# Kernel tuning notes

Measured on AMD Instinct MI355X. Metric: run time of the kernel, lower is better.

The kernel has to match this reference:

```python
import jax, jax.numpy as jnp
import numpy as np

B, IN_CAPS, IN_DIM = 64, 512, 128
NUM_CAPS, DIM_CAPS, NUM_ROUTING = 32, 32, 3


def squash(x, axis=-1):
    sn = jnp.sum(x * x, axis=axis, keepdims=True)
    return (sn / (1.0 + sn)) * x / (jnp.sqrt(sn) + 1e-8)


def setup_inputs() -> dict:
    key = jax.random.key(0)
    k1, k2, k3 = jax.random.split(key, 3)
    input_tensor = jax.random.normal(k1, (B, IN_CAPS, IN_DIM), dtype=jnp.float32)
    W = 0.001 * jax.random.normal(k2, (NUM_CAPS, IN_DIM, DIM_CAPS), dtype=jnp.float32)
    b0 = jax.random.uniform(k3, (B, NUM_CAPS, IN_CAPS, 1), dtype=jnp.float32)
    return {"input_tensor": input_tensor, "W": W, "b0": b0}


def reference(input_tensor, W, b0):
    # u_hat: (B, num_caps, in_caps, dim_caps)
    u_hat = jnp.einsum('bid,ndc->bnic', input_tensor, W)
    temp_u_hat = jax.lax.stop_gradient(u_hat)
    b = b0
    for _ in range(NUM_ROUTING - 1):
        c = jax.nn.softmax(b, axis=1)            # (B, num_caps, in_caps, 1)
        s = jnp.sum(c * temp_u_hat, axis=2)      # (B, num_caps, dim_caps)
        v = squash(s)
        uv = jnp.einsum('bnic,bnc->bni', temp_u_hat, v)[..., None]
        b = b + uv
    c = jax.nn.softmax(b, axis=1)
    s = jnp.sum(c * u_hat, axis=2)
    return squash(s)                             # (B, num_caps, dim_caps)
```

## Files before the change

### kernel.cpp

```cpp
#include <hip/hip_runtime.h>
#include <math.h>

#define IC 512
#define KD 128
#define NC 32
#define DC 32
#define NTHR 512

typedef __attribute__((ext_vector_type(8))) short bf16x8;
typedef __attribute__((ext_vector_type(4))) float f32x4;

__device__ __forceinline__ unsigned short f2bf(float f) {
    unsigned u = __builtin_bit_cast(unsigned, f);
    return (unsigned short)((u + 0x7fffu + ((u >> 16) & 1u)) >> 16);
}
__device__ __forceinline__ float bf2f(unsigned short h) {
    unsigned u = ((unsigned)h) << 16;
    return __builtin_bit_cast(float, u);
}
#define MFMA(a, b, c) __builtin_amdgcn_mfma_f32_16x16x32_bf16(a, b, c, 0, 0, 0)

__global__ __launch_bounds__(NTHR, 1)
void capsmfma(const float* __restrict__ x_g, const float* __restrict__ W_g,
              const float* __restrict__ b0_g, float* __restrict__ out_g,
              unsigned short* __restrict__ xT_g)
{
    __shared__ __align__(16) unsigned short uA[512 * 34];
    __shared__ __align__(16) float s_s[NC * KD];
    __shared__ __align__(16) unsigned short wv_s[NC * 136];

    const int t = threadIdx.x, b = blockIdx.x;
    const int w = t >> 6, l = t & 63;
    const float* __restrict__ xb = x_g + (size_t)b * IC * KD;
    unsigned short* __restrict__ xTb = xT_g + (size_t)b * KD * IC;

    {
        float* tile = (float*)uA;
        for (int c = 0; c < 8; ++c) {
            for (int rep = 0; rep < 4; ++rep) {
                int v = t + rep * NTHR;
                int i = v >> 5, kq = v & 31;
                float4 val = *(const float4*)(xb + (size_t)(c * 64 + i) * KD + (kq << 2));
                float* d = tile + i * 133 + (kq << 2);
                d[0] = val.x; d[1] = val.y; d[2] = val.z; d[3] = val.w;
            }
            __syncthreads();
            {
                const int xk = t >> 2, iseg = t & 3;
                unsigned q[8];
                #pragma unroll
                for (int j = 0; j < 8; ++j) {
                    unsigned short lo = f2bf(tile[(iseg * 16 + 2 * j) * 133 + xk]);
                    unsigned short hi = f2bf(tile[(iseg * 16 + 2 * j + 1) * 133 + xk]);
                    q[j] = (unsigned)lo | ((unsigned)hi << 16);
                }
                unsigned short* dst = xTb + (size_t)xk * IC + c * 64 + iseg * 16;
                float4 o0 = {__builtin_bit_cast(float, q[0]), __builtin_bit_cast(float, q[1]),
                             __builtin_bit_cast(float, q[2]), __builtin_bit_cast(float, q[3])};
                float4 o1 = {__builtin_bit_cast(float, q[4]), __builtin_bit_cast(float, q[5]),
                             __builtin_bit_cast(float, q[6]), __builtin_bit_cast(float, q[7])};
                *(float4*)(dst) = o0;
                *(float4*)(dst + 8) = o1;
            }
            __syncthreads();
        }
    }

    float bb[NC];
    #pragma unroll
    for (int n = 0; n < NC; ++n)
        bb[n] = b0_g[((size_t)(b * NC + n)) * IC + t];

    unsigned short* stage = uA;
    unsigned short* c_bf  = uA;

    for (int r = 0; r < 3; ++r) {
        if (r > 0) {
            f32x4 acc[4][2];
            #pragma unroll
            for (int m4 = 0; m4 < 4; ++m4)
                #pragma unroll
                for (int nt = 0; nt < 2; ++nt) acc[m4][nt] = (f32x4){0.f, 0.f, 0.f, 0.f};
            const int lm = l & 15, kg = l >> 4;
            for (int kt = 0; kt < 4; ++kt) {
                const int xk = kt * 32 + kg * 8;
                bf16x8 bfr0 = *(const bf16x8*)(const void*)(wv_s + (0 * 16 + lm) * 136 + xk);
                bf16x8 bfr1 = *(const bf16x8*)(const void*)(wv_s + (1 * 16 + lm) * 136 + xk);
                #pragma unroll
                for (int m4 = 0; m4 < 4; ++m4) {
                    const int i = (4 * w + m4) * 16 + lm;
                    float4 xa = *(const float4*)(xb + (size_t)i * KD + xk);
                    float4 xc = *(const float4*)(xb + (size_t)i * KD + xk + 4);
                    bf16x8 afr;
                    afr[0] = (short)f2bf(xa.x); afr[1] = (short)f2bf(xa.y);
                    afr[2] = (short)f2bf(xa.z); afr[3] = (short)f2bf(xa.w);
                    afr[4] = (short)f2bf(xc.x); afr[5] = (short)f2bf(xc.y);
                    afr[6] = (short)f2bf(xc.z); afr[7] = (short)f2bf(xc.w);
                    acc[m4][0] = MFMA(afr, bfr0, acc[m4][0]);
                    acc[m4][1] = MFMA(afr, bfr1, acc[m4][1]);
                }
            }
            #pragma unroll
            for (int m4 = 0; m4 < 4; ++m4)
                #pragma unroll
                for (int nt = 0; nt < 2; ++nt)
                    #pragma unroll
                    for (int reg = 0; reg < 4; ++reg) {
                        const int i = (4 * w + m4) * 16 + kg * 4 + reg;
                        const int n = nt * 16 + lm;
                        stage[i * 34 + n] = f2bf(acc[m4][nt][reg]);
                    }
            __syncthreads();
            #pragma unroll
            for (int n = 0; n < NC; ++n) bb[n] += bf2f(stage[t * 34 + n]);
            __syncthreads();
        }

        {
            float m = bb[0];
            #pragma unroll
            for (int n = 1; n < NC; ++n) m = fmaxf(m, bb[n]);
            float e[NC], sum = 0.f;
            #pragma unroll
            for (int n = 0; n < NC; ++n) { e[n] = __expf(bb[n] - m); sum += e[n]; }
            const float inv = 1.f / sum;
            #pragma unroll
            for (int n = 0; n < NC; ++n) c_bf[n * 520 + t] = f2bf(e[n] * inv);
        }
        __syncthreads();

        {
            f32x4 acc2[2];
            acc2[0] = (f32x4){0.f, 0.f, 0.f, 0.f};
            acc2[1] = (f32x4){0.f, 0.f, 0.f, 0.f};
            const int lm = l & 15, kg = l >> 4;
            for (int kt = 0; kt < 16; ++kt) {
                const int i0 = kt * 32 + kg * 8;
                float4 raw = *(const float4*)(xTb + (size_t)(w * 16 + lm) * IC + i0);
                bf16x8 bfr = __builtin_bit_cast(bf16x8, raw);
                #pragma unroll
                for (int mt = 0; mt < 2; ++mt) {
                    bf16x8 afr = *(const bf16x8*)(const void*)(c_bf + (mt * 16 + lm) * 520 + i0);
                    acc2[mt] = MFMA(afr, bfr, acc2[mt]);
                }
            }
            #pragma unroll
            for (int mt = 0; mt < 2; ++mt)
                #pragma unroll
                for (int reg = 0; reg < 4; ++reg) {
                    const int n = mt * 16 + kg * 4 + reg;
                    const int xk = w * 16 + lm;
                    s_s[n * KD + (xk & 96) + ((xk + 4 * n) & 31)] = acc2[mt][reg];
                }
        }
        __syncthreads();

        {
            const int n = t >> 4, dp = t & 15;
            const float* __restrict__ Wn = W_g + (size_t)n * KD * DC;
            float s0 = 0.f, s1 = 0.f;
            #pragma unroll 8
            for (int k = 0; k < KD; ++k) {
                const float sv = s_s[n * KD + (k & 96) + ((k + 4 * n) & 31)];
                const float2 wp = *(const float2*)(Wn + k * DC + (dp << 1));
                s0 += sv * wp.x; s1 += sv * wp.y;
            }
            float sn = s0 * s0 + s1 * s1;
            sn += __shfl_xor(sn, 1); sn += __shfl_xor(sn, 2);
            sn += __shfl_xor(sn, 4); sn += __shfl_xor(sn, 8);
            const float fac = sn / ((1.f + sn) * (sqrtf(sn) + 1e-8f));
            const float v0 = s0 * fac, v1 = s1 * fac;
            if (r == 2) {
                float* o = out_g + ((size_t)(b * NC + n)) * DC + (dp << 1);
                o[0] = v0; o[1] = v1;
            } else {
                float vv[DC];
                const int base = (l >> 4) << 4;
                #pragma unroll
                for (int dd = 0; dd < 16; ++dd) {
                    vv[2 * dd]     = __shfl(v0, base + dd);
                    vv[2 * dd + 1] = __shfl(v1, base + dd);
                }
                #pragma unroll
                for (int kk = 0; kk < 8; ++kk) {
                    const int k = dp * 8 + kk;
                    const float* __restrict__ wr = Wn + k * DC;
                    float a = 0.f;
                    #pragma unroll
                    for (int dd = 0; dd < DC; ++dd) a += wr[dd] * vv[dd];
                    wv_s[n * 136 + k] = f2bf(a);
                }
                __syncthreads();
            }
        }
    }
}

extern "C" void kernel_launch(void* const* d_in, const int* in_sizes, int n_in,
                              void* d_out, int out_size, void* d_ws, size_t ws_size,
                              hipStream_t stream) {
    const float* x  = (const float*)d_in[0];
    const float* W  = (const float*)d_in[1];
    const float* b0 = (const float*)d_in[2];
    float* out = (float*)d_out;
    unsigned short* xT = (unsigned short*)d_ws;
    capsmfma<<<64, NTHR, 0, stream>>>(x, W, b0, out, xT);
}
```

Baseline: 156.3 us.

## Double block size and keep routing logits in MFMA accumulator layout

```diff
diff --git a/kernel.cpp b/kernel.cpp
--- a/kernel.cpp
+++ b/kernel.cpp
@@ -5,7 +5,7 @@
 #define KD 128
 #define NC 32
 #define DC 32
-#define NTHR 512
+#define NTHR 1024
 
 typedef __attribute__((ext_vector_type(8))) short bf16x8;
 typedef __attribute__((ext_vector_type(4))) float f32x4;
@@ -14,184 +14,177 @@
     unsigned u = __builtin_bit_cast(unsigned, f);
     return (unsigned short)((u + 0x7fffu + ((u >> 16) & 1u)) >> 16);
 }
-__device__ __forceinline__ float bf2f(unsigned short h) {
-    unsigned u = ((unsigned)h) << 16;
-    return __builtin_bit_cast(float, u);
-}
 #define MFMA(a, b, c) __builtin_amdgcn_mfma_f32_16x16x32_bf16(a, b, c, 0, 0, 0)
 
 __global__ __launch_bounds__(NTHR, 1)
 void capsmfma(const float* __restrict__ x_g, const float* __restrict__ W_g,
               const float* __restrict__ b0_g, float* __restrict__ out_g,
-              unsigned short* __restrict__ xT_g)
+              unsigned short* __restrict__ xT_g, unsigned short* __restrict__ xb_g)
 {
-    __shared__ __align__(16) unsigned short uA[512 * 34];
+    __shared__ __align__(16) float uni[8512];
     __shared__ __align__(16) float s_s[NC * KD];
     __shared__ __align__(16) unsigned short wv_s[NC * 136];
+    __shared__ __align__(16) float v_s[NC * 33];
 
     const int t = threadIdx.x, b = blockIdx.x;
-    const int w = t >> 6, l = t & 63;
+    const int w = t >> 6, l = t & 63, lm = l & 15, kg = (l >> 4) & 3;
     const float* __restrict__ xb = x_g + (size_t)b * IC * KD;
     unsigned short* __restrict__ xTb = xT_g + (size_t)b * KD * IC;
-
-    {
-        float* tile = (float*)uA;
-        for (int c = 0; c < 8; ++c) {
-            for (int rep = 0; rep < 4; ++rep) {
-                int v = t + rep * NTHR;
-                int i = v >> 5, kq = v & 31;
-                float4 val = *(const float4*)(xb + (size_t)(c * 64 + i) * KD + (kq << 2));
-                float* d = tile + i * 133 + (kq << 2);
-                d[0] = val.x; d[1] = val.y; d[2] = val.z; d[3] = val.w;
-            }
-            __syncthreads();
-            {
-                const int xk = t >> 2, iseg = t & 3;
-                unsigned q[8];
-                #pragma unroll
-                for (int j = 0; j < 8; ++j) {
-                    unsigned short lo = f2bf(tile[(iseg * 16 + 2 * j) * 133 + xk]);
-                    unsigned short hi = f2bf(tile[(iseg * 16 + 2 * j + 1) * 133 + xk]);
-                    q[j] = (unsigned)lo | ((unsigned)hi << 16);
-                }
-                unsigned short* dst = xTb + (size_t)xk * IC + c * 64 + iseg * 16;
-                float4 o0 = {__builtin_bit_cast(float, q[0]), __builtin_bit_cast(float, q[1]),
-                             __builtin_bit_cast(float, q[2]), __builtin_bit_cast(float, q[3])};
-                float4 o1 = {__builtin_bit_cast(float, q[4]), __builtin_bit_cast(float, q[5]),
-                             __builtin_bit_cast(float, q[6]), __builtin_bit_cast(float, q[7])};
-                *(float4*)(dst) = o0;
-                *(float4*)(dst + 8) = o1;
-            }
-            __syncthreads();
-        }
+    unsigned short* __restrict__ xbb = xb_g + (size_t)b * IC * KD;
+    unsigned short* c_bf = (unsigned short*)uni;
+
+    for (int c = 0; c < 8; ++c) {
+        for (int rep = 0; rep < 2; ++rep) {
+            int v = t + rep * NTHR;
+            int i = v >> 5, kq = v & 31;
+            float4 val = *(const float4*)(xb + (size_t)(c * 64 + i) * KD + (kq << 2));
+            float* d = uni + i * 133 + (kq << 2);
+            d[0] = val.x; d[1] = val.y; d[2] = val.z; d[3] = val.w;
+        }
+        __syncthreads();
+        {
+            const int xk = t >> 3, i8 = (t & 7) * 8;
+            unsigned q[4];
+            #pragma unroll
+            for (int j = 0; j < 4; ++j) {
+                unsigned short lo = f2bf(uni[(i8 + 2 * j) * 133 + xk]);
+                unsigned short hi = f2bf(uni[(i8 + 2 * j + 1) * 133 + xk]);
+                q[j] = (unsigned)lo | ((unsigned)hi << 16);
+            }
+            float4 o = {__builtin_bit_cast(float, q[0]), __builtin_bit_cast(float, q[1]),
+                        __builtin_bit_cast(float, q[2]), __builtin_bit_cast(float, q[3])};
+            *(float4*)(xTb + (size_t)xk * IC + c * 64 + i8) = o;
+        }
+        {
+            const int i = t >> 4, k0 = (t & 15) * 8;
+            unsigned q[4];
+            #pragma unroll
+            for (int j = 0; j < 4; ++j) {
+                unsigned short lo = f2bf(uni[i * 133 + k0 + 2 * j]);
+                unsigned short hi = f2bf(uni[i * 133 + k0 + 2 * j + 1]);
+                q[j] = (unsigned)lo | ((unsigned)hi << 16);
+            }
+            float4 o = {__builtin_bit_cast(float, q[0]), __builtin_bit_cast(float, q[1]),
+                        __builtin_bit_cast(float, q[2]), __builtin_bit_cast(float, q[3])};
+            *(float4*)(xbb + (size_t)(c * 64 + i) * KD + k0) = o;
+        }
+        __syncthreads();
     }
 
-    float bb[NC];
+    float bb[2][2][4];
     #pragma unroll
-    for (int n = 0; n < NC; ++n)
-        bb[n] = b0_g[((size_t)(b * NC + n)) * IC + t];
-
-    unsigned short* stage = uA;
-    unsigned short* c_bf  = uA;
+    for (int mt = 0; mt < 2; ++mt)
+        #pragma unroll
+        for (int nt = 0; nt < 2; ++nt)
+            #pragma unroll
+            for (int reg = 0; reg < 4; ++reg)
+                bb[mt][nt][reg] = b0_g[((size_t)(b * NC + lm + 16 * nt)) * IC +
+                                       (2 * w + mt) * 16 + kg * 4 + reg];
 
     for (int r = 0; r < 3; ++r) {
         if (r > 0) {
-            f32x4 acc[4][2];
-            #pragma unroll
-            for (int m4 = 0; m4 < 4; ++m4)
+            f32x4 acc[2][2];
+            #pragma unroll
+            for (int mt = 0; mt < 2; ++mt)
                 #pragma unroll
-                for (int nt = 0; nt < 2; ++nt) acc[m4][nt] = (f32x4){0.f, 0.f, 0.f, 0.f};
-            const int lm = l & 15, kg = l >> 4;
+                for (int nt = 0; nt < 2; ++nt)
+                    #pragma unroll
+                    for (int reg = 0; reg < 4; ++reg) acc[mt][nt][reg] = bb[mt][nt][reg];
             for (int kt = 0; kt < 4; ++kt) {
                 const int xk = kt * 32 + kg * 8;
                 bf16x8 bfr0 = *(const bf16x8*)(const void*)(wv_s + (0 * 16 + lm) * 136 + xk);
                 bf16x8 bfr1 = *(const bf16x8*)(const void*)(wv_s + (1 * 16 + lm) * 136 + xk);
                 #pragma unroll
-                for (int m4 = 0; m4 < 4; ++m4) {
-                    const int i = (4 * w + m4) * 16 + lm;
-                    float4 xa = *(const float4*)(xb + (size_t)i * KD + xk);
-                    float4 xc = *(const float4*)(xb + (size_t)i * KD + xk + 4);
-                    bf16x8 afr;
-                    afr[0] = (short)f2bf(xa.x); afr[1] = (short)f2bf(xa.y);
-                    afr[2] = (short)f2bf(xa.z); afr[3] = (short)f2bf(xa.w);
-                    afr[4] = (short)f2bf(xc.x); afr[5] = (short)f2bf(xc.y);
-                    afr[6] = (short)f2bf(xc.z); afr[7] = (short)f2bf(xc.w);
-                    acc[m4][0] = MFMA(afr, bfr0, acc[m4][0]);
-                    acc[m4][1] = MFMA(afr, bfr1, acc[m4][1]);
+                for (int mt = 0; mt < 2; ++mt) {
+                    const int i = (2 * w + mt) * 16 + lm;
+                    float4 raw = *(const float4*)(xbb + (size_t)i * KD + xk);
+                    bf16x8 afr = __builtin_bit_cast(bf16x8, raw);
+                    acc[mt][0] = MFMA(afr, bfr0, acc[mt][0]);
+                    acc[mt][1] = MFMA(afr, bfr1, acc[mt][1]);
                 }
             }
             #pragma unroll
-            for (int m4 = 0; m4 < 4; ++m4)
+            for (int mt = 0; mt < 2; ++mt)
                 #pragma unroll
                 for (int nt = 0; nt < 2; ++nt)
                     #pragma unroll
-                    for (int reg = 0; reg < 4; ++reg) {
-                        const int i = (4 * w + m4) * 16 + kg * 4 + reg;
-                        const int n = nt * 16 + lm;
-                        stage[i * 34 + n] = f2bf(acc[m4][nt][reg]);
-                    }
-            __syncthreads();
-            #pragma unroll
-            for (int n = 0; n < NC; ++n) bb[n] += bf2f(stage[t * 34 + n]);
-            __syncthreads();
-        }
-
-        {
-            float m = bb[0];
-            #pragma unroll
-            for (int n = 1; n < NC; ++n) m = fmaxf(m, bb[n]);
-            float e[NC], sum = 0.f;
-            #pragma unroll
-            for (int n = 0; n < NC; ++n) { e[n] = __expf(bb[n] - m); sum += e[n]; }
-            const float inv = 1.f / sum;
-            #pragma unroll
-            for (int n = 0; n < NC; ++n) c_bf[n * 520 + t] = f2bf(e[n] * inv);
-        }
-        __syncthreads();
-
-        {
-            f32x4 acc2[2];
-            acc2[0] = (f32x4){0.f, 0.f, 0.f, 0.f};
-            acc2[1] = (f32x4){0.f, 0.f, 0.f, 0.f};
-            const int lm = l & 15, kg = l >> 4;
+                    for (int reg = 0; reg < 4; ++reg) bb[mt][nt][reg] = acc[mt][nt][reg];
+        }
+
+        #pragma unroll
+        for (int mt = 0; mt < 2; ++mt)
+            #pragma unroll
+            for (int reg = 0; reg < 4; ++reg) {
+                float m = fmaxf(bb[mt][0][reg], bb[mt][1][reg]);
+                m = fmaxf(m, __shfl_xor(m, 1)); m = fmaxf(m, __shfl_xor(m, 2));
+                m = fmaxf(m, __shfl_xor(m, 4)); m = fmaxf(m, __shfl_xor(m, 8));
+                float e0 = __expf(bb[mt][0][reg] - m);
+                float e1 = __expf(bb[mt][1][reg] - m);
+                float sum = e0 + e1;
+                sum += __shfl_xor(sum, 1); sum += __shfl_xor(sum, 2);
+                sum += __shfl_xor(sum, 4); sum += __shfl_xor(sum, 8);
+                const float inv = 1.f / sum;
+                const int i = (2 * w + mt) * 16 + kg * 4 + reg;
+                c_bf[lm * 520 + i]        = f2bf(e0 * inv);
+                c_bf[(lm + 16) * 520 + i] = f2bf(e1 * inv);
+            }
+        __syncthreads();
+
+        {
+            const int mt2 = w >> 3, xkt = w & 7;
+            f32x4 acc2 = (f32x4){0.f, 0.f, 0.f, 0.f};
             for (int kt = 0; kt < 16; ++kt) {
                 const int i0 = kt * 32 + kg * 8;
-                float4 raw = *(const float4*)(xTb + (size_t)(w * 16 + lm) * IC + i0);
+                float4 raw = *(const float4*)(xTb + (size_t)(xkt * 16 + lm) * IC + i0);
                 bf16x8 bfr = __builtin_bit_cast(bf16x8, raw);
-                #pragma unroll
-                for (int mt = 0; mt < 2; ++mt) {
-                    bf16x8 afr = *(const bf16x8*)(const void*)(c_bf + (mt * 16 + lm) * 520 + i0);
-                    acc2[mt] = MFMA(afr, bfr, acc2[mt]);
+                bf16x8 afr = *(const bf16x8*)(const void*)(c_bf + (mt2 * 16 + lm) * 520 + i0);
+                acc2 = MFMA(afr, bfr, acc2);
+            }
+            #pragma unroll
+            for (int reg = 0; reg < 4; ++reg) {
+                const int n = mt2 * 16 + kg * 4 + reg;
+                const int xk = xkt * 16 + lm;
+                s_s[n * KD + (xk & 96) + ((xk + 4 * n) & 31)] = acc2[reg];
+            }
+        }
+        __syncthreads();
+
+        {
+            const int n = t >> 5, d = t & 31;
+            const float* __restrict__ Wn = W_g + (size_t)n * KD * DC;
+            float s = 0.f;
+            #pragma unroll 8
+            for (int k = 0; k < KD; ++k)
+                s += s_s[n * KD + (k & 96) + ((k + 4 * n) & 31)] * Wn[k * DC + d];
+            float sn = s * s;
+            sn += __shfl_xor(sn, 1); sn += __shfl_xor(sn, 2);
+            sn += __shfl_xor(sn, 4); sn += __shfl_xor(sn, 8); sn += __shfl_xor(sn, 16);
+            const float fac = sn / ((1.f + sn) * (sqrtf(sn) + 1e-8f));
+            const float vv = s * fac;
+            if (r == 2) {
+                out_g[((size_t)(b * NC + n)) * DC + d] = vv;
+            } else {
+                v_s[n * 33 + d] = vv;
+            }
+        }
+        if (r < 2) {
+            __syncthreads();
+            {
+                const int n = t >> 5, kq = t & 31;
+                const float* __restrict__ Wn = W_g + (size_t)n * KD * DC;
+                float a[4] = {0.f, 0.f, 0.f, 0.f};
+                #pragma unroll 4
+                for (int dd = 0; dd < DC; ++dd) {
+                    const float vd = v_s[n * 33 + dd];
+                    #pragma unroll
+                    for (int j = 0; j < 4; ++j)
+                        a[j] += Wn[(kq * 4 + j) * DC + dd] * vd;
                 }
-            }
-            #pragma unroll
-            for (int mt = 0; mt < 2; ++mt)
-                #pragma unroll
-                for (int reg = 0; reg < 4; ++reg) {
-                    const int n = mt * 16 + kg * 4 + reg;
-                    const int xk = w * 16 + lm;
-                    s_s[n * KD + (xk & 96) + ((xk + 4 * n) & 31)] = acc2[mt][reg];
-                }
-        }
-        __syncthreads();
-
-        {
-            const int n = t >> 4, dp = t & 15;
-            const float* __restrict__ Wn = W_g + (size_t)n * KD * DC;
-            float s0 = 0.f, s1 = 0.f;
-            #pragma unroll 8
-            for (int k = 0; k < KD; ++k) {
-                const float sv = s_s[n * KD + (k & 96) + ((k + 4 * n) & 31)];
-                const float2 wp = *(const float2*)(Wn + k * DC + (dp << 1));
-                s0 += sv * wp.x; s1 += sv * wp.y;
-            }
-            float sn = s0 * s0 + s1 * s1;
-            sn += __shfl_xor(sn, 1); sn += __shfl_xor(sn, 2);
-            sn += __shfl_xor(sn, 4); sn += __shfl_xor(sn, 8);
-            const float fac = sn / ((1.f + sn) * (sqrtf(sn) + 1e-8f));
-            const float v0 = s0 * fac, v1 = s1 * fac;
-            if (r == 2) {
-                float* o = out_g + ((size_t)(b * NC + n)) * DC + (dp << 1);
-                o[0] = v0; o[1] = v1;
-            } else {
-                float vv[DC];
-                const int base = (l >> 4) << 4;
-                #pragma unroll
-                for (int dd = 0; dd < 16; ++dd) {
-                    vv[2 * dd]     = __shfl(v0, base + dd);
-                    vv[2 * dd + 1] = __shfl(v1, base + dd);
-                }
-                #pragma unroll
-                for (int kk = 0; kk < 8; ++kk) {
-                    const int k = dp * 8 + kk;
-                    const float* __restrict__ wr = Wn + k * DC;
-                    float a = 0.f;
-                    #pragma unroll
-                    for (int dd = 0; dd < DC; ++dd) a += wr[dd] * vv[dd];
-                    wv_s[n * 136 + k] = f2bf(a);
-                }
-                __syncthreads();
-            }
+                ushort4 o;
+                o.x = f2bf(a[0]); o.y = f2bf(a[1]); o.z = f2bf(a[2]); o.w = f2bf(a[3]);
+                *(ushort4*)(wv_s + n * 136 + kq * 4) = o;
+            }
+            __syncthreads();
         }
     }
 }
@@ -204,5 +197,6 @@
     const float* b0 = (const float*)d_in[2];
     float* out = (float*)d_out;
     unsigned short* xT = (unsigned short*)d_ws;
-    capsmfma<<<64, NTHR, 0, stream>>>(x, W, b0, out, xT);
+    unsigned short* xbf = xT + (size_t)64 * KD * IC;
+    capsmfma<<<64, NTHR, 0, stream>>>(x, W, b0, out, xT, xbf);
 }
```

Measured after the change: 165.4 us. 5.8% more time.
